# Optimization experiments

Measured on AMD Instinct MI355X. Metric: run time of the kernel, lower is better.

Reference implementation:

```python
import jax, jax.numpy as jnp
import numpy as np

B, T, V, F, O, K_ORDER = 16, 16, 512, 64, 64, 3


def setup_inputs() -> dict:
    key = jax.random.key(0)
    k1, k2, k3, k4 = jax.random.split(key, 4)
    x = jax.random.normal(k1, (B, T, V, F), dtype=jnp.float32)
    Att = jax.random.uniform(k2, (B, V, V), dtype=jnp.float32)
    S = jax.random.uniform(k3, (B, T, V, V), dtype=jnp.float32)
    Theta = jax.random.uniform(k4, (K_ORDER, F, O), dtype=jnp.float32) * 0.1
    return {"x": x, "Att": Att, "S": S, "Theta": Theta}


def reference(x, Att, S, Theta):
    # x: (B,T,V,F); Att: (B,V,V); S: (B,T,V,V); Theta: (k,F,O)
    Bv, Tv, Vv, Fv = x.shape
    k_order = Theta.shape[0]
    # symmetrize via elementwise min with transpose over the two vertex dims
    S = jnp.minimum(S, jnp.swapaxes(S, -1, -2))
    # per-timestep: D = diag(sum(A, axis=1)) (sum over rows, i.e. axis=2 here)
    deg = S.sum(axis=2)                      # (B,T,V)
    eye = jnp.eye(Vv, dtype=x.dtype)
    # L_t = D - A - I
    L_t = deg[..., None] * eye - S - eye     # (B,T,V,V)
    Att_b = Att[:, None]                     # (B,1,V,V) broadcast over T

    # Chebyshev recurrence is ELEMENTWISE in the original code: T_k = 2*L_t*T_{k-1} - T_{k-2}
    Tkm2 = jnp.broadcast_to(eye, L_t.shape)  # T_0 = I
    Tkm1 = L_t                               # T_1 = L_t
    # rhs = (T_k * Att)^T @ x  ->  sum_u (T_k*Att)[u,v] * x[u,f]; then @ Theta[k]
    out = jnp.einsum('btuv,btuf,fo->btvo', Tkm2 * Att_b, x, Theta[0])
    if k_order > 1:
        out = out + jnp.einsum('btuv,btuf,fo->btvo', Tkm1 * Att_b, x, Theta[1])
    for i in range(2, k_order):
        Tk = 2.0 * L_t * Tkm1 - Tkm2
        out = out + jnp.einsum('btuv,btuf,fo->btvo', Tk * Att_b, x, Theta[i])
        Tkm2, Tkm1 = Tkm1, Tk
    return jax.nn.relu(out)                  # (B,T,V,O)
```

## Files before the change

### kernel.cpp

```cpp
#include <hip/hip_runtime.h>

#define VV 512
#define FF 64
#define OO 64
#define YELEMS 8388608

#define C1_OFF    0u
#define C2_OFF    67108864u
#define Y1F8_OFF  134217728u
#define Y2F8_OFF  142606336u
#define YVO_OFF   150994944u
#define DEGP_OFF  201326592u
#define SDG_OFF   205520896u
#define ADG_OFF   206045184u
#define WS_NEED   206569472u

using f32x4  = __attribute__((ext_vector_type(4))) float;
using f32x16 = __attribute__((ext_vector_type(16))) float;
using s16x8  = __attribute__((ext_vector_type(8))) short;
using s16x4  = __attribute__((ext_vector_type(4))) short;
using u16x4  = __attribute__((ext_vector_type(4))) unsigned short;
using i64x2  = __attribute__((ext_vector_type(2))) long;

__device__ __forceinline__ short f2bf(float f) {
    union { float f; unsigned int u; } v; v.f = f;
    unsigned int u = v.u;
    u += 0x7fffu + ((u >> 16) & 1u);
    return (short)(u >> 16);
}
__device__ __forceinline__ float bf2f(unsigned short u) {
    union { unsigned int u; float f; } v; v.u = ((unsigned int)u) << 16; return v.f;
}
__device__ __forceinline__ int swz(int row) { return (row >> 1) & 7; }

__device__ __forceinline__ void gload16(const void* g, void* l) {
    __builtin_amdgcn_global_load_lds(
        (const __attribute__((address_space(1))) unsigned int*)g,
        (__attribute__((address_space(3))) unsigned int*)l, 16, 0, 0);
}

__global__ __launch_bounds__(256, 4)
void att_kernel(const float* __restrict__ Att, unsigned char* __restrict__ ws)
{
    __shared__ float T[64][65];
    const int tid = threadIdx.x;
    const int b  = blockIdx.x >> 6;
    const int ij = blockIdx.x & 63;
    const int i = ij >> 3, j = ij & 7;
    const float* Ab = Att + (size_t)b * VV * VV;
    const int r = tid >> 2, c4 = (tid & 3) * 16;
    const float* src = Ab + (size_t)(i * 64 + r) * VV + j * 64 + c4;
    #pragma unroll
    for (int w = 0; w < 4; ++w) {
        float4 t = ((const float4*)src)[w];
        T[r][c4 + w * 4 + 0] = t.x; T[r][c4 + w * 4 + 1] = t.y;
        T[r][c4 + w * 4 + 2] = t.z; T[r][c4 + w * 4 + 3] = t.w;
    }
    __syncthreads();
    unsigned short* dst = (unsigned short*)(ws + Y1F8_OFF) + (size_t)b * (VV * VV)
                        + (size_t)(j * 64 + r) * VV + i * 64 + c4;
    s16x8 p0, p1;
    #pragma unroll
    for (int e = 0; e < 8; ++e) {
        p0[e] = f2bf(T[c4 + e][r]);
        p1[e] = f2bf(T[c4 + 8 + e][r]);
    }
    *(s16x8*)dst = p0;
    *(s16x8*)(dst + 8) = p1;
}

__global__ __launch_bounds__(256, 4)
void coef_kernel(const float* __restrict__ S, const float* __restrict__ Att,
                 unsigned char* __restrict__ ws)
{
    __shared__ float Sij[64][65];
    __shared__ float Sji[64][65];

    const int tid = threadIdx.x;
    const int bt = blockIdx.x / 36;
    int p = blockIdx.x - bt * 36;
    int i = 0;
    while (p >= 8 - i) { p -= 8 - i; ++i; }
    const int j = i + p;
    const int b = bt >> 4;
    const int u0i = i * 64, u0j = j * 64;

    const float* Sbt = S + (size_t)bt * VV * VV;
    const float* Abt = Att + (size_t)b * VV * VV;
    const unsigned short* atT = (const unsigned short*)(ws + Y1F8_OFF) + (size_t)b * (VV * VV);

    {
        const int r = tid >> 2, c4 = (tid & 3) * 16;
        const float* gij = Sbt + (size_t)(u0i + r) * VV + u0j + c4;
        const float* gji = Sbt + (size_t)(u0j + r) * VV + u0i + c4;
        #pragma unroll
        for (int w = 0; w < 4; ++w) {
            float4 t = ((const float4*)gij)[w];
            Sij[r][c4 + w * 4 + 0] = t.x; Sij[r][c4 + w * 4 + 1] = t.y;
            Sij[r][c4 + w * 4 + 2] = t.z; Sij[r][c4 + w * 4 + 3] = t.w;
        }
        #pragma unroll
        for (int w = 0; w < 4; ++w) {
            float4 t = ((const float4*)gji)[w];
            Sji[r][c4 + w * 4 + 0] = t.x; Sji[r][c4 + w * 4 + 1] = t.y;
            Sji[r][c4 + w * 4 + 2] = t.z; Sji[r][c4 + w * 4 + 3] = t.w;
        }
    }
    if (i == j && tid < 64) {
        const int vg = u0i + tid;
        ((float*)(ws + SDG_OFF))[(size_t)bt * VV + vg] = Sbt[(size_t)vg * VV + vg];
        ((float*)(ws + ADG_OFF))[(size_t)bt * VV + vg] = Abt[(size_t)vg * VV + vg];
    }
    __syncthreads();

    unsigned char* c1w = ws + C1_OFF + (size_t)bt * (VV * VV);
    unsigned char* c2w = ws + C2_OFF + (size_t)bt * (VV * VV);
    float* degpW = (float*)(ws + DEGP_OFF) + (size_t)bt * 8 * VV;

    const int v  = tid >> 2;
    const int sp = tid & 3;
    const int pr = sp >> 1, idx = sp & 1;

    #pragma unroll
    for (int pass = 0; pass < 2; ++pass) {
        if (pass == 1 && i == j) break;
        const float (*Tuv)[65] = (pass == 0) ? Sij : Sji;
        const float (*Tvu)[65] = (pass == 0) ? Sji : Sij;
        const int I = (pass == 0) ? i : j;
        const int J = (pass == 0) ? j : i;
        const bool dtile = (i == j);

        const unsigned short* arow = atT + (size_t)(J * 64 + v) * VV + I * 64;

        float degp = 0.f;
        int w1[4], w2[4];
        #pragma unroll
        for (int t = 0; t < 2; ++t) {
            const int sl = idx * 4 + t * 2 + pr;
            s16x8 a8 = *(const s16x8*)(arow + sl * 8);
            float c1v[8], c2v[8];
            #pragma unroll
            for (int e = 0; e < 8; ++e) {
                const int u = sl * 8 + e;
                float sm = fminf(Tuv[u][v], Tvu[v][u]);
                float a  = bf2f((unsigned short)a8[e]);
                degp += sm;
                float c1 = -a * sm;
                float c2 = (a + a) * (sm * sm);
                if (dtile && (u == v)) { c1 = 0.f; c2 = 0.f; }
                c1v[e] = c1; c2v[e] = c2;
            }
            int a0 = __builtin_amdgcn_cvt_pk_fp8_f32(c1v[0], c1v[1], 0, false);
            a0     = __builtin_amdgcn_cvt_pk_fp8_f32(c1v[2], c1v[3], a0, true);
            int a1 = __builtin_amdgcn_cvt_pk_fp8_f32(c1v[4], c1v[5], 0, false);
            a1     = __builtin_amdgcn_cvt_pk_fp8_f32(c1v[6], c1v[7], a1, true);
            int b0 = __builtin_amdgcn_cvt_pk_fp8_f32(c2v[0], c2v[1], 0, false);
            b0     = __builtin_amdgcn_cvt_pk_fp8_f32(c2v[2], c2v[3], b0, true);
            int b1 = __builtin_amdgcn_cvt_pk_fp8_f32(c2v[4], c2v[5], 0, false);
            b1     = __builtin_amdgcn_cvt_pk_fp8_f32(c2v[6], c2v[7], b1, true);
            w1[t * 2] = a0; w1[t * 2 + 1] = a1;
            w2[t * 2] = b0; w2[t * 2 + 1] = b1;
        }
        const int vglob = J * 64 + v;
        const size_t rowoff = (size_t)vglob * VV + pr * 256 + I * 32 + idx * 16;
        int4 s1 = { w1[0], w1[1], w1[2], w1[3] };
        int4 s2 = { w2[0], w2[1], w2[2], w2[3] };
        *(int4*)(c1w + rowoff) = s1;
        *(int4*)(c2w + rowoff) = s2;

        degp += __shfl_xor(degp, 1);
        degp += __shfl_xor(degp, 2);
        if (sp == 0) degpW[(size_t)I * VV + vglob] = degp;
    }
}

__global__ __launch_bounds__(256, 4)
void y_kernel2(const float* __restrict__ x, const float* __restrict__ Theta,
               unsigned char* __restrict__ ws)
{
    __shared__ __align__(16) unsigned char smem[32768];
    short* xT = (short*)(smem);

    const int tid = threadIdx.x, lane = tid & 63, q = tid >> 6;
    const int g = lane >> 4, nbase = lane & 15;
    const int bt = blockIdx.x >> 3;
    const int u0 = (blockIdx.x & 7) * 64;

    {
        const float* xp = x + ((size_t)(bt * VV + u0 + lane)) * FF + q * 16;
        float4 a0 = ((const float4*)xp)[0];
        float4 a1 = ((const float4*)xp)[1];
        float4 a2 = ((const float4*)xp)[2];
        float4 a3 = ((const float4*)xp)[3];
        float v[16] = {a0.x,a0.y,a0.z,a0.w, a1.x,a1.y,a1.z,a1.w,
                       a2.x,a2.y,a2.z,a2.w, a3.x,a3.y,a3.z,a3.w};
        s16x8 p0, p1;
        #pragma unroll
        for (int e = 0; e < 8; ++e) { p0[e] = f2bf(v[e]); p1[e] = f2bf(v[8 + e]); }
        const int fs = swz(lane);
        *(s16x8*)&xT[lane * 64 + (((q * 2)     ^ fs) * 8)] = p0;
        *(s16x8*)&xT[lane * 64 + (((q * 2 + 1) ^ fs) * 8)] = p1;
    }
    #pragma unroll
    for (int k = 0; k < 3; ++k) {
        short* tk = (short*)(smem + 8192 + k * 8192);
        s16x8 p0, p1;
        #pragma unroll
        for (int e = 0; e < 8; ++e) {
            p0[e] = f2bf(Theta[k * FF * OO + (q * 16 + e) * OO + lane]);
            p1[e] = f2bf(Theta[k * FF * OO + (q * 16 + 8 + e) * OO + lane]);
        }
        const int fs = swz(lane);
        *(s16x8*)&tk[lane * 64 + (((q * 2)     ^ fs) * 8)] = p0;
        *(s16x8*)&tk[lane * 64 + (((q * 2 + 1) ^ fs) * 8)] = p1;
    }
    __syncthreads();

    f32x4 zero = {0.f, 0.f, 0.f, 0.f};
    f32x4 acc[3][4];
    #pragma unroll
    for (int k = 0; k < 3; ++k)
        #pragma unroll
        for (int nt = 0; nt < 4; ++nt) acc[k][nt] = zero;

    const int mrow = q * 16 + nbase;
    const int moff = mrow * 64, ms = swz(mrow);
    #pragma unroll
    for (int kk = 0; kk < 2; ++kk) {
        const int slotA = kk * 4 + g;
        s16x8 a = *(const s16x8*)&xT[moff + ((slotA ^ ms) * 8)];
        #pragma unroll
        for (int nt = 0; nt < 4; ++nt) {
            const int nrow = nt * 16 + nbase;
            const int nad = nrow * 64 + ((slotA ^ swz(nrow)) * 8);
            #pragma unroll
            for (int k = 0; k < 3; ++k) {
                s16x8 bb = *(const s16x8*)&((short*)(smem + 8192 + k * 8192))[nad];
                acc[k][nt] = __builtin_amdgcn_mfma_f32_16x16x32_bf16(a, bb, acc[k][nt], 0, 0, 0);
            }
        }
    }
    unsigned short* yvo = (unsigned short*)(ws + YVO_OFF);
    unsigned char* y1f8 = ws + Y1F8_OFF + (size_t)bt * 32768;
    unsigned char* y2f8 = ws + Y2F8_OFF + (size_t)bt * 32768;
    #pragma unroll
    for (int k = 0; k < 3; ++k) {
        #pragma unroll
        for (int nt = 0; nt < 4; ++nt) {
            const int o = nt * 16 + nbase;
            const int u = u0 + q * 16 + g * 4;
            #pragma unroll
            for (int r = 0; r < 4; ++r)
                yvo[(size_t)k * YELEMS + (size_t)bt * 32768 + (size_t)(u + r) * OO + o] =
                    (unsigned short)f2bf(acc[k][nt][r]);
            if (k >= 1) {
                const int s = u >> 3;
                const int sw = (s & ~15) | ((s & 15) ^ (o & 15));
                const int ad = o * 512 + sw * 8 + (u & 4);
                int w = __builtin_amdgcn_cvt_pk_fp8_f32(acc[k][nt][0], acc[k][nt][1], 0, false);
                w     = __builtin_amdgcn_cvt_pk_fp8_f32(acc[k][nt][2], acc[k][nt][3], w, true);
                if (k == 1) *(int*)(y1f8 + ad) = w;
                else        *(int*)(y2f8 + ad) = w;
            }
        }
    }
}

__global__ __launch_bounds__(256, 2)
void cheb_b(const unsigned char* __restrict__ ws, float* __restrict__ out)
{
    __shared__ __align__(16) unsigned char yLds[65536];

    const int tid = threadIdx.x, lane = tid & 63;
    const int wv = tid >> 6;
    const int vh = wv >> 1, oh = wv & 1;
    const int rl = lane & 31, hi = lane >> 5;

    const int wg = blockIdx.x;
    const int bt = (wg & 7) + ((wg >> 6) << 3);
    const int vt = (wg >> 3) & 7;
    const int v0 = vt * 64;

    {
        const unsigned char* y1img = ws + Y1F8_OFF + (size_t)bt * 32768;
        const unsigned char* y2img = ws + Y2F8_OFF + (size_t)bt * 32768;
        const int wo = wv * 1024 + lane * 16;
        #pragma unroll
        for (int i = 0; i < 8; ++i) {
            gload16(y1img + i * 4096 + wo, (char*)yLds + i * 4096 + wv * 1024);
            gload16(y2img + i * 4096 + wo, (char*)yLds + 32768 + i * 4096 + wv * 1024);
        }
    }

    const size_t crow = (size_t)(v0 + vh * 32 + rl) * VV + hi * 256;
    const unsigned char* c1base = ws + C1_OFF + (size_t)bt * (VV * VV) + crow;
    const unsigned char* c2base = ws + C2_OFF + (size_t)bt * (VV * VV) + crow;
    i64x2 c1p[16], c2p[16];
    #pragma unroll
    for (int jj = 0; jj < 16; ++jj) {
        c1p[jj] = *(const i64x2*)(c1base + jj * 16);
        c2p[jj] = *(const i64x2*)(c2base + jj * 16);
    }

    __syncthreads();

    f32x16 acc;
    #pragma unroll
    for (int i = 0; i < 16; ++i) acc[i] = 0.f;

    const int yrow = (oh * 32 + rl) * 512;
    const int x15  = rl & 15;

    #pragma unroll
    for (int it = 0; it < 32; ++it) {
        const long a1 = c1p[it >> 1][it & 1];
        const long a2 = c2p[it >> 1][it & 1];
        const int s  = it * 2 + hi;
        const int sw = (s & ~15) | ((s & 15) ^ x15);
        const int ad = yrow + sw * 8;
        const long b1 = *(const long*)&yLds[ad];
        const long b2 = *(const long*)&yLds[32768 + ad];
        acc = __builtin_amdgcn_mfma_f32_32x32x16_fp8_fp8(a1, b1, acc, 0, 0, 0);
        acc = __builtin_amdgcn_mfma_f32_32x32x16_fp8_fp8(a2, b2, acc, 0, 0, 0);
    }

    __syncthreads();
    {
        float* ep = (float*)yLds;
        const float* degp = (const float*)(ws + DEGP_OFF) + (size_t)bt * 8 * VV;
        const float* SdgW = (const float*)(ws + SDG_OFF) + (size_t)bt * VV;
        const float* AdgW = (const float*)(ws + ADG_OFF) + (size_t)bt * VV;
        if (tid < 64) {
            float dv = 0.f;
            #pragma unroll
            for (int s = 0; s < 8; ++s) dv += degp[(size_t)s * VV + v0 + tid];
            ep[tid] = dv;
        } else if (tid < 128) {
            ep[64 + (tid - 64)] = SdgW[v0 + (tid - 64)];
        } else if (tid < 192) {
            ep[128 + (tid - 128)] = AdgW[v0 + (tid - 128)];
        }
    }
    __syncthreads();

    const float* ep = (const float*)yLds;
    const unsigned short* yvo = (const unsigned short*)(ws + YVO_OFF) + (size_t)bt * 32768;
    float* obt = out + (size_t)bt * VV * OO;
    const int o = oh * 32 + rl;

    #pragma unroll
    for (int r = 0; r < 16; ++r) {
        const int vloc = vh * 32 + (r & 3) + 8 * (r >> 2) + 4 * hi;
        const int vgr = v0 + vloc;
        const float dv = ep[vloc];
        const float Sd = ep[64 + vloc];
        const float Ad = ep[128 + vloc];
        const float Ld = dv - Sd - 1.0f;
        const float w1 = Ad * Ld;
        const float w2 = Ad * (2.0f * Ld * Ld - 1.0f);
        const size_t yi = (size_t)vgr * OO + o;
        float y0v = bf2f(yvo[yi]);
        float y1v = bf2f(yvo[(size_t)YELEMS + yi]);
        float y2v = bf2f(yvo[(size_t)2 * YELEMS + yi]);
        float val = acc[r] + Ad * y0v + w1 * y1v + w2 * y2v;
        obt[(size_t)vgr * OO + o] = fmaxf(val, 0.0f);
    }
}

__global__ __launch_bounds__(256, 4)
void y_kernel_fb(const float* __restrict__ x, const float* __restrict__ Theta,
                 unsigned short* __restrict__ yT)
{
    __shared__ __align__(16) unsigned char smem[32768];
    short* xT = (short*)(smem);
    const int tid = threadIdx.x, lane = tid & 63, q = tid >> 6;
    const int g = lane >> 4, nbase = lane & 15;
    const int bt = blockIdx.x >> 3;
    const int u0 = (blockIdx.x & 7) * 64;
    {
        const float* xp = x + ((size_t)(bt * VV + u0 + lane)) * FF + q * 16;
        float4 a0 = ((const float4*)xp)[0];
        float4 a1 = ((const float4*)xp)[1];
        float4 a2 = ((const float4*)xp)[2];
        float4 a3 = ((const float4*)xp)[3];
        float v[16] = {a0.x,a0.y,a0.z,a0.w, a1.x,a1.y,a1.z,a1.w,
                       a2.x,a2.y,a2.z,a2.w, a3.x,a3.y,a3.z,a3.w};
        s16x8 p0, p1;
        #pragma unroll
        for (int e = 0; e < 8; ++e) { p0[e] = f2bf(v[e]); p1[e] = f2bf(v[8 + e]); }
        const int fs = swz(lane);
        *(s16x8*)&xT[lane * 64 + (((q * 2)     ^ fs) * 8)] = p0;
        *(s16x8*)&xT[lane * 64 + (((q * 2 + 1) ^ fs) * 8)] = p1;
    }
    #pragma unroll
    for (int k = 0; k < 3; ++k) {
        short* tk = (short*)(smem + 8192 + k * 8192);
        s16x8 p0, p1;
        #pragma unroll
        for (int e = 0; e < 8; ++e) {
            p0[e] = f2bf(Theta[k * FF * OO + (q * 16 + e) * OO + lane]);
            p1[e] = f2bf(Theta[k * FF * OO + (q * 16 + 8 + e) * OO + lane]);
        }
        const int fs = swz(lane);
        *(s16x8*)&tk[lane * 64 + (((q * 2)     ^ fs) * 8)] = p0;
        *(s16x8*)&tk[lane * 64 + (((q * 2 + 1) ^ fs) * 8)] = p1;
    }
    __syncthreads();
    f32x4 zero = {0.f, 0.f, 0.f, 0.f};
    f32x4 acc[3][4];
    #pragma unroll
    for (int k = 0; k < 3; ++k)
        #pragma unroll
        for (int nt = 0; nt < 4; ++nt) acc[k][nt] = zero;
    const int mrow = q * 16 + nbase;
    const int moff = mrow * 64, ms = swz(mrow);
    #pragma unroll
    for (int kk = 0; kk < 2; ++kk) {
        const int slotA = kk * 4 + g;
        s16x8 a = *(const s16x8*)&xT[moff + ((slotA ^ ms) * 8)];
        #pragma unroll
        for (int nt = 0; nt < 4; ++nt) {
            const int nrow = nt * 16 + nbase;
            const int nad = nrow * 64 + ((slotA ^ swz(nrow)) * 8);
            #pragma unroll
            for (int k = 0; k < 3; ++k) {
                s16x8 bb = *(const s16x8*)&((short*)(smem + 8192 + k * 8192))[nad];
                acc[k][nt] = __builtin_amdgcn_mfma_f32_16x16x32_bf16(a, bb, acc[k][nt], 0, 0, 0);
            }
        }
    }
    #pragma unroll
    for (int k = 0; k < 3; ++k) {
        #pragma unroll
        for (int nt = 0; nt < 4; ++nt) {
            const int o = nt * 16 + nbase;
            const int u = u0 + q * 16 + g * 4;
            u16x4 pk;
            #pragma unroll
            for (int r = 0; r < 4; ++r) pk[r] = (unsigned short)f2bf(acc[k][nt][r]);
            *(u16x4*)&yT[(size_t)k * YELEMS + ((size_t)(bt * 64 + o)) * VV + u] = pk;
        }
    }
}

__global__ __launch_bounds__(256, 4)
void cheb_main_fb(const float* __restrict__ S, const float* __restrict__ Att,
                  const unsigned short* __restrict__ yT, float* __restrict__ out)
{
    const int tid = threadIdx.x, lane = tid & 63, q = tid >> 6;
    const int g = lane >> 4, nbase = lane & 15;
    const int wg = blockIdx.x;
    const int bt = (wg & 7) + ((wg >> 6) << 3);
    const int vt = (wg >> 3) & 7;
    const int v0 = vt * 64;
    const int b  = bt >> 4;
    const float* Sbt = S + (size_t)bt * VV * VV;
    const float* Abt = Att + (size_t)b * VV * VV;
    const unsigned short* y0g = yT + (size_t)bt * 64 * VV;
    const unsigned short* y1g = y0g + (size_t)YELEMS;
    const unsigned short* y2g = y0g + (size_t)2 * YELEMS;
    const int mrow = q * 16 + nbase;
    const int vg   = v0 + mrow;
    const float* Srow = Sbt + (size_t)vg * VV;
    const float* Scol = Sbt + vg;
    const float* Acol = Abt + vg;
    f32x4 zero = {0.f, 0.f, 0.f, 0.f};
    f32x4 acc[4];
    #pragma unroll
    for (int i = 0; i < 4; ++i) acc[i] = zero;
    float da0 = 0.f, da1 = 0.f, adg = 0.f, sdg = 0.f;
    #pragma unroll
    for (int ut = 0; ut < 8; ++ut) {
        const int u0t = ut * 64;
        #pragma unroll
        for (int kk = 0; kk < 2; ++kk) {
            const int ub = u0t + (kk * 4 + g) * 8;
            s16x8 b10 = *(const s16x8*)&y1g[(size_t)(0 * 16 + nbase) * VV + ub];
            s16x8 b11 = *(const s16x8*)&y1g[(size_t)(1 * 16 + nbase) * VV + ub];
            s16x8 b12 = *(const s16x8*)&y1g[(size_t)(2 * 16 + nbase) * VV + ub];
            s16x8 b13 = *(const s16x8*)&y1g[(size_t)(3 * 16 + nbase) * VV + ub];
            f32x4 r0 = *(const f32x4*)(Srow + ub);
            f32x4 r1 = *(const f32x4*)(Srow + ub + 4);
            s16x8 a1, a2;
            #pragma unroll
            for (int e = 0; e < 8; ++e) {
                float sc = Scol[(size_t)(ub + e) * VV];
                float av = Acol[(size_t)(ub + e) * VV];
                float rv = (e < 4) ? r0[e] : r1[e - 4];
                float sm = fminf(sc, rv);
                if (e & 1) da1 += sm; else da0 += sm;
                float c1 = -av * sm;
                float c2 = (av + av) * (sm * sm);
                if (ub + e == vg) { c1 = 0.f; c2 = 0.f; adg = av; sdg = sm; }
                a1[e] = f2bf(c1);
                a2[e] = f2bf(c2);
            }
            acc[0] = __builtin_amdgcn_mfma_f32_16x16x32_bf16(a1, b10, acc[0], 0, 0, 0);
            acc[1] = __builtin_amdgcn_mfma_f32_16x16x32_bf16(a1, b11, acc[1], 0, 0, 0);
            acc[2] = __builtin_amdgcn_mfma_f32_16x16x32_bf16(a1, b12, acc[2], 0, 0, 0);
            acc[3] = __builtin_amdgcn_mfma_f32_16x16x32_bf16(a1, b13, acc[3], 0, 0, 0);
            s16x8 b20 = *(const s16x8*)&y2g[(size_t)(0 * 16 + nbase) * VV + ub];
            s16x8 b21 = *(const s16x8*)&y2g[(size_t)(1 * 16 + nbase) * VV + ub];
            s16x8 b22 = *(const s16x8*)&y2g[(size_t)(2 * 16 + nbase) * VV + ub];
            s16x8 b23 = *(const s16x8*)&y2g[(size_t)(3 * 16 + nbase) * VV + ub];
            acc[0] = __builtin_amdgcn_mfma_f32_16x16x32_bf16(a2, b20, acc[0], 0, 0, 0);
            acc[1] = __builtin_amdgcn_mfma_f32_16x16x32_bf16(a2, b21, acc[1], 0, 0, 0);
            acc[2] = __builtin_amdgcn_mfma_f32_16x16x32_bf16(a2, b22, acc[2], 0, 0, 0);
            acc[3] = __builtin_amdgcn_mfma_f32_16x16x32_bf16(a2, b23, acc[3], 0, 0, 0);
        }
    }
    float da = da0 + da1;
    da  += __shfl_xor(da, 16);  da  += __shfl_xor(da, 32);
    adg += __shfl_xor(adg, 16); adg += __shfl_xor(adg, 32);
    sdg += __shfl_xor(sdg, 16); sdg += __shfl_xor(sdg, 32);
    float* obt = out + (size_t)bt * VV * OO;
    #pragma unroll
    for (int r = 0; r < 4; ++r) {
        const int vloc = q * 16 + g * 4 + r;
        const int src  = g * 4 + r;
        const float Ad = __shfl(adg, src);
        const float dv = __shfl(da,  src);
        const float Sd = __shfl(sdg, src);
        const float Ld = dv - Sd - 1.0f;
        const float w1 = Ad * Ld;
        const float w2 = Ad * (2.0f * Ld * Ld - 1.0f);
        const int vgr = v0 + vloc;
        #pragma unroll
        for (int nt = 0; nt < 4; ++nt) {
            const int oo = nt * 16 + nbase;
            const size_t yi = (size_t)oo * VV + vgr;
            float y0v = bf2f(y0g[yi]);
            float y1v = bf2f(y1g[yi]);
            float y2v = bf2f(y2g[yi]);
            float val = acc[nt][r] + Ad * y0v + w1 * y1v + w2 * y2v;
            obt[(size_t)vgr * OO + oo] = fmaxf(val, 0.0f);
        }
    }
}

extern "C" void kernel_launch(void* const* d_in, const int* in_sizes, int n_in,
                              void* d_out, int out_size, void* d_ws, size_t ws_size,
                              hipStream_t stream) {
    (void)in_sizes; (void)n_in; (void)out_size;
    const float* x   = (const float*)d_in[0];
    const float* Att = (const float*)d_in[1];
    const float* S   = (const float*)d_in[2];
    const float* Th  = (const float*)d_in[3];
    float* outp = (float*)d_out;
    if (ws_size >= (size_t)WS_NEED) {
        unsigned char* ws = (unsigned char*)d_ws;
        hipLaunchKernelGGL(att_kernel, dim3(1024), dim3(256), 0, stream, Att, ws);
        hipLaunchKernelGGL(coef_kernel, dim3(9216), dim3(256), 0, stream, S, Att, ws);
        hipLaunchKernelGGL(y_kernel2, dim3(2048), dim3(256), 0, stream, x, Th, ws);
        hipLaunchKernelGGL(cheb_b, dim3(2048), dim3(256), 0, stream, ws, outp);
    } else {
        unsigned short* yT = (unsigned short*)d_ws;
        hipLaunchKernelGGL(y_kernel_fb, dim3(2048), dim3(256), 0, stream, x, Th, yT);
        hipLaunchKernelGGL(cheb_main_fb, dim3(2048), dim3(256), 0, stream, S, Att, yT, outp);
    }
}
```

Baseline: 224.0 us.

## Restructure coef kernel to per-row blocks reading S columns directly without LDS

The coefficient kernel now assigns one block per (bt, 64-row strip) instead of per symmetric tile pair. Each lane handles one vertex row and reads both the row and the column of S straight from global memory, dropping the LDS transpose tiles and the triangular tile indexing. Degree partials are reduced to 4 slices instead of 8, and the consumer is updated to match. The strided column reads (stride VV floats per lane, coalesced across lanes) replace the tiled transpose, and S is now read twice overall instead of once.

```diff
diff --git a/kernel.cpp b/kernel.cpp
--- a/kernel.cpp
+++ b/kernel.cpp
@@ -69,109 +69,93 @@
     *(s16x8*)(dst + 8) = p1;
 }
 
-__global__ __launch_bounds__(256, 4)
+__global__ __launch_bounds__(256, 6)
 void coef_kernel(const float* __restrict__ S, const float* __restrict__ Att,
                  unsigned char* __restrict__ ws)
 {
-    __shared__ float Sij[64][65];
-    __shared__ float Sji[64][65];
-
-    const int tid = threadIdx.x;
-    const int bt = blockIdx.x / 36;
-    int p = blockIdx.x - bt * 36;
-    int i = 0;
-    while (p >= 8 - i) { p -= 8 - i; ++i; }
-    const int j = i + p;
-    const int b = bt >> 4;
-    const int u0i = i * 64, u0j = j * 64;
+    const int tid = threadIdx.x, lane = tid & 63, Q = tid >> 6;
+
+    const int wg = blockIdx.x;
+    const int bt = (wg & 7) + ((wg >> 6) << 3);
+    const int vt = (wg >> 3) & 7;
+    const int v0 = vt * 64;
+    const int b  = bt >> 4;
+    const int v  = v0 + lane;
 
     const float* Sbt = S + (size_t)bt * VV * VV;
     const float* Abt = Att + (size_t)b * VV * VV;
-    const unsigned short* atT = (const unsigned short*)(ws + Y1F8_OFF) + (size_t)b * (VV * VV);
-
-    {
-        const int r = tid >> 2, c4 = (tid & 3) * 16;
-        const float* gij = Sbt + (size_t)(u0i + r) * VV + u0j + c4;
-        const float* gji = Sbt + (size_t)(u0j + r) * VV + u0i + c4;
-        #pragma unroll
-        for (int w = 0; w < 4; ++w) {
-            float4 t = ((const float4*)gij)[w];
-            Sij[r][c4 + w * 4 + 0] = t.x; Sij[r][c4 + w * 4 + 1] = t.y;
-            Sij[r][c4 + w * 4 + 2] = t.z; Sij[r][c4 + w * 4 + 3] = t.w;
-        }
-        #pragma unroll
-        for (int w = 0; w < 4; ++w) {
-            float4 t = ((const float4*)gji)[w];
-            Sji[r][c4 + w * 4 + 0] = t.x; Sji[r][c4 + w * 4 + 1] = t.y;
-            Sji[r][c4 + w * 4 + 2] = t.z; Sji[r][c4 + w * 4 + 3] = t.w;
-        }
-    }
-    if (i == j && tid < 64) {
-        const int vg = u0i + tid;
-        ((float*)(ws + SDG_OFF))[(size_t)bt * VV + vg] = Sbt[(size_t)vg * VV + vg];
-        ((float*)(ws + ADG_OFF))[(size_t)bt * VV + vg] = Abt[(size_t)vg * VV + vg];
-    }
-    __syncthreads();
-
-    unsigned char* c1w = ws + C1_OFF + (size_t)bt * (VV * VV);
-    unsigned char* c2w = ws + C2_OFF + (size_t)bt * (VV * VV);
+    const unsigned short* arow = (const unsigned short*)(ws + Y1F8_OFF)
+                               + (size_t)b * (VV * VV) + (size_t)v * VV;
+    const float* srow = Sbt + (size_t)v * VV;
+    const float* scol = Sbt + v;
+
+    unsigned char* c1r = ws + C1_OFF + (size_t)bt * (VV * VV) + (size_t)v * VV;
+    unsigned char* c2r = ws + C2_OFF + (size_t)bt * (VV * VV) + (size_t)v * VV;
     float* degpW = (float*)(ws + DEGP_OFF) + (size_t)bt * 8 * VV;
 
-    const int v  = tid >> 2;
-    const int sp = tid & 3;
-    const int pr = sp >> 1, idx = sp & 1;
-
-    #pragma unroll
-    for (int pass = 0; pass < 2; ++pass) {
-        if (pass == 1 && i == j) break;
-        const float (*Tuv)[65] = (pass == 0) ? Sij : Sji;
-        const float (*Tvu)[65] = (pass == 0) ? Sji : Sij;
-        const int I = (pass == 0) ? i : j;
-        const int J = (pass == 0) ? j : i;
-        const bool dtile = (i == j);
-
-        const unsigned short* arow = atT + (size_t)(J * 64 + v) * VV + I * 64;
-
-        float degp = 0.f;
-        int w1[4], w2[4];
-        #pragma unroll
-        for (int t = 0; t < 2; ++t) {
-            const int sl = idx * 4 + t * 2 + pr;
-            s16x8 a8 = *(const s16x8*)(arow + sl * 8);
-            float c1v[8], c2v[8];
-            #pragma unroll
-            for (int e = 0; e < 8; ++e) {
-                const int u = sl * 8 + e;
-                float sm = fminf(Tuv[u][v], Tvu[v][u]);
-                float a  = bf2f((unsigned short)a8[e]);
-                degp += sm;
-                float c1 = -a * sm;
-                float c2 = (a + a) * (sm * sm);
-                if (dtile && (u == v)) { c1 = 0.f; c2 = 0.f; }
-                c1v[e] = c1; c2v[e] = c2;
+    if (tid < 64) {
+        ((float*)(ws + SDG_OFF))[(size_t)bt * VV + v] = Sbt[(size_t)v * VV + v];
+        ((float*)(ws + ADG_OFF))[(size_t)bt * VV + v] = Abt[(size_t)v * VV + v];
+    }
+
+    const int ub0 = Q * 128;
+    float deg = 0.f;
+
+    #pragma unroll
+    for (int par = 0; par < 2; ++par) {
+        #pragma unroll
+        for (int pp = 0; pp < 4; ++pp) {
+            const int bu = ub0 + par * 8 + pp * 32;
+            float sc[16];
+            #pragma unroll
+            for (int o = 0; o < 2; ++o)
+                #pragma unroll
+                for (int e = 0; e < 8; ++e)
+                    sc[o * 8 + e] = scol[(size_t)(bu + o * 16 + e) * VV];
+            f32x4 r0 = *(const f32x4*)(srow + bu);
+            f32x4 r1 = *(const f32x4*)(srow + bu + 4);
+            f32x4 r2 = *(const f32x4*)(srow + bu + 16);
+            f32x4 r3 = *(const f32x4*)(srow + bu + 20);
+            s16x8 a0 = *(const s16x8*)(arow + bu);
+            s16x8 a1v = *(const s16x8*)(arow + bu + 16);
+
+            int w1[4], w2[4];
+            #pragma unroll
+            for (int o = 0; o < 2; ++o) {
+                float c1v[8], c2v[8];
+                #pragma unroll
+                for (int e = 0; e < 8; ++e) {
+                    const int u = bu + o * 16 + e;
+                    float rv = (o == 0) ? ((e < 4) ? r0[e] : r1[e - 4])
+                                        : ((e < 4) ? r2[e] : r3[e - 4]);
+                    float a  = bf2f((unsigned short)((o == 0) ? a0[e] : a1v[e]));
+                    float sm = fminf(sc[o * 8 + e], rv);
+                    deg += sm;
+                    float c1 = -a * sm;
+                    float c2 = (a + a) * (sm * sm);
+                    if (u == v) { c1 = 0.f; c2 = 0.f; }
+                    c1v[e] = c1; c2v[e] = c2;
+                }
+                int p0 = __builtin_amdgcn_cvt_pk_fp8_f32(c1v[0], c1v[1], 0, false);
+                p0     = __builtin_amdgcn_cvt_pk_fp8_f32(c1v[2], c1v[3], p0, true);
+                int p1 = __builtin_amdgcn_cvt_pk_fp8_f32(c1v[4], c1v[5], 0, false);
+                p1     = __builtin_amdgcn_cvt_pk_fp8_f32(c1v[6], c1v[7], p1, true);
+                int q0 = __builtin_amdgcn_cvt_pk_fp8_f32(c2v[0], c2v[1], 0, false);
+                q0     = __builtin_amdgcn_cvt_pk_fp8_f32(c2v[2], c2v[3], q0, true);
+                int q1 = __builtin_amdgcn_cvt_pk_fp8_f32(c2v[4], c2v[5], 0, false);
+                q1     = __builtin_amdgcn_cvt_pk_fp8_f32(c2v[6], c2v[7], q1, true);
+                w1[o * 2] = p0; w1[o * 2 + 1] = p1;
+                w2[o * 2] = q0; w2[o * 2 + 1] = q1;
             }
-            int a0 = __builtin_amdgcn_cvt_pk_fp8_f32(c1v[0], c1v[1], 0, false);
-            a0     = __builtin_amdgcn_cvt_pk_fp8_f32(c1v[2], c1v[3], a0, true);
-            int a1 = __builtin_amdgcn_cvt_pk_fp8_f32(c1v[4], c1v[5], 0, false);
-            a1     = __builtin_amdgcn_cvt_pk_fp8_f32(c1v[6], c1v[7], a1, true);
-            int b0 = __builtin_amdgcn_cvt_pk_fp8_f32(c2v[0], c2v[1], 0, false);
-            b0     = __builtin_amdgcn_cvt_pk_fp8_f32(c2v[2], c2v[3], b0, true);
-            int b1 = __builtin_amdgcn_cvt_pk_fp8_f32(c2v[4], c2v[5], 0, false);
-            b1     = __builtin_amdgcn_cvt_pk_fp8_f32(c2v[6], c2v[7], b1, true);
-            w1[t * 2] = a0; w1[t * 2 + 1] = a1;
-            w2[t * 2] = b0; w2[t * 2 + 1] = b1;
-        }
-        const int vglob = J * 64 + v;
-        const size_t rowoff = (size_t)vglob * VV + pr * 256 + I * 32 + idx * 16;
-        int4 s1 = { w1[0], w1[1], w1[2], w1[3] };
-        int4 s2 = { w2[0], w2[1], w2[2], w2[3] };
-        *(int4*)(c1w + rowoff) = s1;
-        *(int4*)(c2w + rowoff) = s2;
-
-        degp += __shfl_xor(degp, 1);
-        degp += __shfl_xor(degp, 2);
-        if (sp == 0) degpW[(size_t)I * VV + vglob] = degp;
-    }
+            const int du = par * 256 + ((bu >> 4) * 8);
+            int4 s1 = { w1[0], w1[1], w1[2], w1[3] };
+            int4 s2 = { w2[0], w2[1], w2[2], w2[3] };
+            *(int4*)(c1r + du) = s1;
+            *(int4*)(c2r + du) = s2;
+        }
+    }
+
+    degpW[(size_t)Q * VV + v] = deg;
 }
 
 __global__ __launch_bounds__(256, 4)
@@ -333,7 +317,7 @@
         if (tid < 64) {
             float dv = 0.f;
             #pragma unroll
-            for (int s = 0; s < 8; ++s) dv += degp[(size_t)s * VV + v0 + tid];
+            for (int s = 0; s < 4; ++s) dv += degp[(size_t)s * VV + v0 + tid];
             ep[tid] = dv;
         } else if (tid < 128) {
             ep[64 + (tid - 64)] = SdgW[v0 + (tid - 64)];
@@ -550,7 +534,7 @@
     if (ws_size >= (size_t)WS_NEED) {
         unsigned char* ws = (unsigned char*)d_ws;
         hipLaunchKernelGGL(att_kernel, dim3(1024), dim3(256), 0, stream, Att, ws);
-        hipLaunchKernelGGL(coef_kernel, dim3(9216), dim3(256), 0, stream, S, Att, ws);
+        hipLaunchKernelGGL(coef_kernel, dim3(2048), dim3(256), 0, stream, S, Att, ws);
         hipLaunchKernelGGL(y_kernel2, dim3(2048), dim3(256), 0, stream, x, Th, ws);
         hipLaunchKernelGGL(cheb_b, dim3(2048), dim3(256), 0, stream, ws, outp);
     } else {
```

Measured after the change: 532.7 us. +137.8%, slower.

## Make coef kernel persistent per timestep with double-buffered tile prefetch

Applied to the files above, without the earlier changes.

The coef kernel now runs one 512-thread block per half of a (b,t) slice, looping over 18 tile pairs instead of launching one block per pair. The next pair's S tiles and Att row are loaded into registers while the current pair is computed, then written into a second LDS buffer. The aim is to hide global-load latency and cut per-block launch and setup cost. In exchange only 512 blocks run, which lowers occupancy and parallelism across the GPU. Each iteration also adds two barriers and uses more LDS.

```diff
diff --git a/kernel.cpp b/kernel.cpp
--- a/kernel.cpp
+++ b/kernel.cpp
@@ -37,6 +37,12 @@
     __builtin_amdgcn_global_load_lds(
         (const __attribute__((address_space(1))) unsigned int*)g,
         (__attribute__((address_space(3))) unsigned int*)l, 16, 0, 0);
+}
+
+__device__ __forceinline__ void pair_decode(int p, int& i, int& j) {
+    i = 0;
+    while (p >= 8 - i) { p -= 8 - i; ++i; }
+    j = i + p;
 }
 
 __global__ __launch_bounds__(256, 4)
@@ -69,108 +75,134 @@
     *(s16x8*)(dst + 8) = p1;
 }
 
-__global__ __launch_bounds__(256, 4)
+__global__ __launch_bounds__(512, 4)
 void coef_kernel(const float* __restrict__ S, const float* __restrict__ Att,
                  unsigned char* __restrict__ ws)
 {
-    __shared__ float Sij[64][65];
-    __shared__ float Sji[64][65];
+    __shared__ float buf[2][2][64][65];
 
     const int tid = threadIdx.x;
-    const int bt = blockIdx.x / 36;
-    int p = blockIdx.x - bt * 36;
-    int i = 0;
-    while (p >= 8 - i) { p -= 8 - i; ++i; }
-    const int j = i + p;
+    const int bt   = blockIdx.x >> 1;
+    const int half = blockIdx.x & 1;
     const int b = bt >> 4;
-    const int u0i = i * 64, u0j = j * 64;
 
     const float* Sbt = S + (size_t)bt * VV * VV;
     const float* Abt = Att + (size_t)b * VV * VV;
-    const unsigned short* atT = (const unsigned short*)(ws + Y1F8_OFF) + (size_t)b * (VV * VV);
-
-    {
-        const int r = tid >> 2, c4 = (tid & 3) * 16;
-        const float* gij = Sbt + (size_t)(u0i + r) * VV + u0j + c4;
-        const float* gji = Sbt + (size_t)(u0j + r) * VV + u0i + c4;
-        #pragma unroll
-        for (int w = 0; w < 4; ++w) {
-            float4 t = ((const float4*)gij)[w];
-            Sij[r][c4 + w * 4 + 0] = t.x; Sij[r][c4 + w * 4 + 1] = t.y;
-            Sij[r][c4 + w * 4 + 2] = t.z; Sij[r][c4 + w * 4 + 3] = t.w;
-        }
-        #pragma unroll
-        for (int w = 0; w < 4; ++w) {
-            float4 t = ((const float4*)gji)[w];
-            Sji[r][c4 + w * 4 + 0] = t.x; Sji[r][c4 + w * 4 + 1] = t.y;
-            Sji[r][c4 + w * 4 + 2] = t.z; Sji[r][c4 + w * 4 + 3] = t.w;
-        }
-    }
-    if (i == j && tid < 64) {
-        const int vg = u0i + tid;
-        ((float*)(ws + SDG_OFF))[(size_t)bt * VV + vg] = Sbt[(size_t)vg * VV + vg];
-        ((float*)(ws + ADG_OFF))[(size_t)bt * VV + vg] = Abt[(size_t)vg * VV + vg];
-    }
-    __syncthreads();
+    const unsigned short* atT = (const unsigned short*)(ws + Y1F8_OFF)
+                              + (size_t)b * (VV * VV);
 
     unsigned char* c1w = ws + C1_OFF + (size_t)bt * (VV * VV);
     unsigned char* c2w = ws + C2_OFF + (size_t)bt * (VV * VV);
     float* degpW = (float*)(ws + DEGP_OFF) + (size_t)bt * 8 * VV;
 
-    const int v  = tid >> 2;
-    const int sp = tid & 3;
-    const int pr = sp >> 1, idx = sp & 1;
-
-    #pragma unroll
-    for (int pass = 0; pass < 2; ++pass) {
-        if (pass == 1 && i == j) break;
-        const float (*Tuv)[65] = (pass == 0) ? Sij : Sji;
-        const float (*Tvu)[65] = (pass == 0) ? Sji : Sij;
-        const int I = (pass == 0) ? i : j;
-        const int J = (pass == 0) ? j : i;
-        const bool dtile = (i == j);
-
-        const unsigned short* arow = atT + (size_t)(J * 64 + v) * VV + I * 64;
-
-        float degp = 0.f;
-        int w1[4], w2[4];
-        #pragma unroll
-        for (int t = 0; t < 2; ++t) {
-            const int sl = idx * 4 + t * 2 + pr;
-            s16x8 a8 = *(const s16x8*)(arow + sl * 8);
+    const int r  = tid >> 3;
+    const int cq = tid & 7;
+    const int v  = r;
+    const int sp = tid & 7;
+    const int pr = sp >> 2;
+    const int jsl = sp & 3;
+    const int s_oct = 2 * jsl + pr;
+
+    const int p0 = half * 18;
+
+    int ic, jc;
+    pair_decode(p0, ic, jc);
+    {
+        const float* gij = Sbt + (size_t)(ic * 64 + r) * VV + jc * 64 + cq * 8;
+        const float* gji = Sbt + (size_t)(jc * 64 + r) * VV + ic * 64 + cq * 8;
+        f32x4 t0 = *(const f32x4*)(gij);
+        f32x4 t1 = *(const f32x4*)(gij + 4);
+        f32x4 t2 = *(const f32x4*)(gji);
+        f32x4 t3 = *(const f32x4*)(gji + 4);
+        #pragma unroll
+        for (int k = 0; k < 4; ++k) {
+            buf[0][0][r][cq * 8 + k]     = t0[k];
+            buf[0][0][r][cq * 8 + 4 + k] = t1[k];
+            buf[0][1][r][cq * 8 + k]     = t2[k];
+            buf[0][1][r][cq * 8 + 4 + k] = t3[k];
+        }
+    }
+    s16x8 a0c = *(const s16x8*)(atT + (size_t)(jc * 64 + v) * VV + ic * 64 + s_oct * 8);
+    s16x8 a1c = *(const s16x8*)(atT + (size_t)(ic * 64 + v) * VV + jc * 64 + s_oct * 8);
+    __syncthreads();
+
+    for (int it = 0; it < 18; ++it) {
+        const int cur = it & 1;
+        int in_, jn;
+        pair_decode(p0 + ((it < 17) ? it + 1 : it), in_, jn);
+        const float* gij = Sbt + (size_t)(in_ * 64 + r) * VV + jn * 64 + cq * 8;
+        const float* gji = Sbt + (size_t)(jn * 64 + r) * VV + in_ * 64 + cq * 8;
+        f32x4 n0 = *(const f32x4*)(gij);
+        f32x4 n1 = *(const f32x4*)(gij + 4);
+        f32x4 n2 = *(const f32x4*)(gji);
+        f32x4 n3 = *(const f32x4*)(gji + 4);
+        s16x8 a0n = *(const s16x8*)(atT + (size_t)(jn * 64 + v) * VV + in_ * 64 + s_oct * 8);
+        s16x8 a1n = *(const s16x8*)(atT + (size_t)(in_ * 64 + v) * VV + jn * 64 + s_oct * 8);
+
+        if (ic == jc && sp == 0) {
+            const int vg = ic * 64 + v;
+            ((float*)(ws + SDG_OFF))[(size_t)bt * VV + vg] = Sbt[(size_t)vg * VV + vg];
+            ((float*)(ws + ADG_OFF))[(size_t)bt * VV + vg] = Abt[(size_t)vg * VV + vg];
+        }
+
+        #pragma unroll
+        for (int pass = 0; pass < 2; ++pass) {
+            if (pass == 1 && ic == jc) break;
+            const float (*Tuv)[65] = (pass == 0) ? buf[cur][0] : buf[cur][1];
+            const float (*Tvu)[65] = (pass == 0) ? buf[cur][1] : buf[cur][0];
+            const int I = (pass == 0) ? ic : jc;
+            const int J = (pass == 0) ? jc : ic;
+            const s16x8 a8 = (pass == 0) ? a0c : a1c;
+            const bool dtile = (ic == jc);
+
+            float degp = 0.f;
             float c1v[8], c2v[8];
             #pragma unroll
             for (int e = 0; e < 8; ++e) {
-                const int u = sl * 8 + e;
-                float sm = fminf(Tuv[u][v], Tvu[v][u]);
+                const int ul = s_oct * 8 + e;
+                float su = Tuv[ul][v];
+                float rv = Tvu[v][ul];
                 float a  = bf2f((unsigned short)a8[e]);
+                float sm = fminf(su, rv);
                 degp += sm;
                 float c1 = -a * sm;
                 float c2 = (a + a) * (sm * sm);
-                if (dtile && (u == v)) { c1 = 0.f; c2 = 0.f; }
+                if (dtile && (ul == v)) { c1 = 0.f; c2 = 0.f; }
                 c1v[e] = c1; c2v[e] = c2;
             }
-            int a0 = __builtin_amdgcn_cvt_pk_fp8_f32(c1v[0], c1v[1], 0, false);
-            a0     = __builtin_amdgcn_cvt_pk_fp8_f32(c1v[2], c1v[3], a0, true);
-            int a1 = __builtin_amdgcn_cvt_pk_fp8_f32(c1v[4], c1v[5], 0, false);
-            a1     = __builtin_amdgcn_cvt_pk_fp8_f32(c1v[6], c1v[7], a1, true);
-            int b0 = __builtin_amdgcn_cvt_pk_fp8_f32(c2v[0], c2v[1], 0, false);
-            b0     = __builtin_amdgcn_cvt_pk_fp8_f32(c2v[2], c2v[3], b0, true);
-            int b1 = __builtin_amdgcn_cvt_pk_fp8_f32(c2v[4], c2v[5], 0, false);
-            b1     = __builtin_amdgcn_cvt_pk_fp8_f32(c2v[6], c2v[7], b1, true);
-            w1[t * 2] = a0; w1[t * 2 + 1] = a1;
-            w2[t * 2] = b0; w2[t * 2 + 1] = b1;
-        }
-        const int vglob = J * 64 + v;
-        const size_t rowoff = (size_t)vglob * VV + pr * 256 + I * 32 + idx * 16;
-        int4 s1 = { w1[0], w1[1], w1[2], w1[3] };
-        int4 s2 = { w2[0], w2[1], w2[2], w2[3] };
-        *(int4*)(c1w + rowoff) = s1;
-        *(int4*)(c2w + rowoff) = s2;
-
-        degp += __shfl_xor(degp, 1);
-        degp += __shfl_xor(degp, 2);
-        if (sp == 0) degpW[(size_t)I * VV + vglob] = degp;
+            int w1a = __builtin_amdgcn_cvt_pk_fp8_f32(c1v[0], c1v[1], 0, false);
+            w1a     = __builtin_amdgcn_cvt_pk_fp8_f32(c1v[2], c1v[3], w1a, true);
+            int w1b = __builtin_amdgcn_cvt_pk_fp8_f32(c1v[4], c1v[5], 0, false);
+            w1b     = __builtin_amdgcn_cvt_pk_fp8_f32(c1v[6], c1v[7], w1b, true);
+            int w2a = __builtin_amdgcn_cvt_pk_fp8_f32(c2v[0], c2v[1], 0, false);
+            w2a     = __builtin_amdgcn_cvt_pk_fp8_f32(c2v[2], c2v[3], w2a, true);
+            int w2b = __builtin_amdgcn_cvt_pk_fp8_f32(c2v[4], c2v[5], 0, false);
+            w2b     = __builtin_amdgcn_cvt_pk_fp8_f32(c2v[6], c2v[7], w2b, true);
+
+            const int vglob = J * 64 + v;
+            const size_t off = (size_t)vglob * VV + pr * 256 + I * 32 + jsl * 8;
+            int2 s1; s1.x = w1a; s1.y = w1b;
+            int2 s2; s2.x = w2a; s2.y = w2b;
+            *(int2*)(c1w + off) = s1;
+            *(int2*)(c2w + off) = s2;
+
+            degp += __shfl_xor(degp, 1);
+            degp += __shfl_xor(degp, 2);
+            degp += __shfl_xor(degp, 4);
+            if (sp == 0) degpW[(size_t)I * VV + vglob] = degp;
+        }
+
+        __syncthreads();
+        #pragma unroll
+        for (int k = 0; k < 4; ++k) {
+            buf[cur ^ 1][0][r][cq * 8 + k]     = n0[k];
+            buf[cur ^ 1][0][r][cq * 8 + 4 + k] = n1[k];
+            buf[cur ^ 1][1][r][cq * 8 + k]     = n2[k];
+            buf[cur ^ 1][1][r][cq * 8 + 4 + k] = n3[k];
+        }
+        __syncthreads();
+        ic = in_; jc = jn;
+        a0c = a0n; a1c = a1n;
     }
 }
 
@@ -550,7 +582,7 @@
     if (ws_size >= (size_t)WS_NEED) {
         unsigned char* ws = (unsigned char*)d_ws;
         hipLaunchKernelGGL(att_kernel, dim3(1024), dim3(256), 0, stream, Att, ws);
-        hipLaunchKernelGGL(coef_kernel, dim3(9216), dim3(256), 0, stream, S, Att, ws);
+        hipLaunchKernelGGL(coef_kernel, dim3(512), dim3(512), 0, stream, S, Att, ws);
         hipLaunchKernelGGL(y_kernel2, dim3(2048), dim3(256), 0, stream, x, Th, ws);
         hipLaunchKernelGGL(cheb_b, dim3(2048), dim3(256), 0, stream, ws, outp);
     } else {
```

Result: slower. 244.7 us (+9.2%).
